# Kernel tuning notes

Hardware: AMD Instinct MI355X
Metric: run time of the kernel (lower is better)

Reference implementation:

```python
import jax, jax.numpy as jnp
import numpy as np

EMBED_DIM = 32
HIDDEN_DIM = 64
N = 1024
LN_EPS = 1e-5


def setup_inputs() -> dict:
    key = jax.random.key(0)
    ks = jax.random.split(key, 8)
    d, h = EMBED_DIM, HIDDEN_DIM
    s1 = 1.0 / np.sqrt(2 * d)
    s2 = 1.0 / np.sqrt(h)
    return {
        "node_embeddings": jax.random.normal(ks[0], (N, d), dtype=jnp.float32),
        # Linear(2d -> h), stored as (2d, h) for x @ W
        "W1": jax.random.uniform(ks[1], (2 * d, h), jnp.float32, -s1, s1),
        "b1": jnp.zeros((h,), jnp.float32),
        "g1": jnp.ones((h,), jnp.float32),
        "be1": jnp.zeros((h,), jnp.float32),
        "W2": jax.random.uniform(ks[2], (h, h), jnp.float32, -s2, s2),
        "b2": jnp.zeros((h,), jnp.float32),
        "g2": jnp.ones((h,), jnp.float32),
        "be2": jnp.zeros((h,), jnp.float32),
        "W3": jax.random.uniform(ks[3], (h, 1), jnp.float32, -s2, s2),
        "b3": jnp.zeros((1,), jnp.float32),
    }


def _layernorm(x, gamma, beta):
    mu = jnp.mean(x, axis=-1, keepdims=True)
    var = jnp.mean(jnp.square(x - mu), axis=-1, keepdims=True)
    return (x - mu) * jax.lax.rsqrt(var + LN_EPS) * gamma + beta


def reference(node_embeddings, W1, b1, g1, be1, W2, b2, g2, be2, W3, b3):
    n, d = node_embeddings.shape
    # pair_emb = cat([src_emb, dst_emb], -1); first linear applied without
    # materializing the concat: split W1 into src/dst halves.
    W1s, W1d = W1[:d], W1[d:]
    hs = node_embeddings @ W1s          # (N, h)
    hd = node_embeddings @ W1d          # (N, h)
    h = hs[:, None, :] + hd[None, :, :] + b1   # (N, N, h)
    h = jax.nn.relu(_layernorm(h, g1, be1))
    h = jax.nn.relu(_layernorm(h @ W2 + b2, g2, be2))
    out = jax.nn.sigmoid((h @ W3 + b3)[..., 0])  # (N, N)
    return out
```

## Files before the change

kernel.cpp:

```cpp
#include <hip/hip_runtime.h>
#include <hip/hip_bf16.h>

#define NN 1024
#define ED 32
#define HD 64
#define LN_EPS 1e-5f

typedef short bf16x8 __attribute__((ext_vector_type(8)));
typedef float f32x4 __attribute__((ext_vector_type(4)));

#define OFF_HS   0
#define OFF_HDB  65536
#define OFF_SS   131072
#define OFF_SD   132096
#define OFF_G1   133120
#define OFF_BE1  133184
#define OFF_B2   133248
#define OFF_G2   133312
#define OFF_BE2  133376
#define OFF_W3   133440
#define OFF_B3   133504
#define OFF_SB2  133505
#define OFF_W2F  133508

__device__ __forceinline__ bool buf_is_f32(const void* g1) {
  return *(const unsigned int*)g1 == 0x3F800000u;
}
template <bool F32>
__device__ __forceinline__ float ld(const void* p, int i) {
  return F32 ? ((const float*)p)[i]
             : __bfloat162float(((const __hip_bfloat16*)p)[i]);
}
__device__ __forceinline__ unsigned short f2bf(float f) {
  unsigned int b = __builtin_bit_cast(unsigned int, f);
  b += 0x7FFFu + ((b >> 16) & 1u);
  return (unsigned short)(b >> 16);
}
__device__ __forceinline__ unsigned int pack2bf(float a, float b) {
  return (unsigned int)f2bf(a) | ((unsigned int)f2bf(b) << 16);
}
__device__ __forceinline__ unsigned int pk_bf(float a, float b) {
  __hip_bfloat162 p = __float22bfloat162_rn(make_float2(a, b));
  unsigned int u;
  __builtin_memcpy(&u, &p, 4);
  return u;
}
__device__ __forceinline__ f32x4 splat4(float v) { f32x4 r = {v, v, v, v}; return r; }

template <int CTRL>
__device__ __forceinline__ float dpp_add(float v) {
  int m = __builtin_amdgcn_update_dpp(0, __builtin_bit_cast(int, v), CTRL, 0xF, 0xF, true);
  return v + __builtin_bit_cast(float, m);
}
__device__ __forceinline__ float red16(float v) {
  v = dpp_add<0xB1>(v);
  v = dpp_add<0x4E>(v);
  v = dpp_add<0x124>(v);
  v = dpp_add<0x128>(v);
  return v;
}

template <bool F32>
__device__ void prep_body(const void* E, const void* W1, const void* b1,
                          const void* g1, const void* be1, const void* W2,
                          const void* b2, const void* g2, const void* be2,
                          const void* W3, const void* b3, float* ws) {
  const int i = blockIdx.x, t = threadIdx.x;
  if (i < NN) {
    __shared__ float e[ED];
    if (t < ED) e[t] = ld<F32>(E, i * ED + t);
    __syncthreads();
    int k = t & 63;
    bool dside = t >= 64;
    int wofs = dside ? ED * HD : 0;
    float acc = 0.f;
#pragma unroll
    for (int c = 0; c < ED; ++c)
      acc = fmaf(e[c], ld<F32>(W1, wofs + c * HD + k), acc);
    if (dside) acc += ld<F32>(b1, k);
    float s = acc;
#pragma unroll
    for (int m = 1; m <= 32; m <<= 1) s += __shfl_xor(s, m);
    if (dside) {
      ws[OFF_HDB + i * HD + k] = acc;
      if (k == 0) ws[OFF_SD + i] = s;
    } else {
      ws[OFF_HS + i * HD + k] = acc;
      if (k == 0) ws[OFF_SS + i] = s;
    }
  } else if (i < NN + 16) {
    if (t < 32) {
      int d = (i - NN) * 32 + t;
      int lv = d & 63, nt = (d >> 6) & 3, kc = d >> 8;
      int k0 = kc * 32 + ((lv >> 4) & 3) * 8;
      int n = nt * 16 + (lv & 15);
      unsigned int u4[4];
#pragma unroll
      for (int jj = 0; jj < 4; ++jj)
        u4[jj] = pack2bf(ld<F32>(W2, (k0 + 2 * jj) * HD + n),
                         ld<F32>(W2, (k0 + 2 * jj + 1) * HD + n));
      ((uint4*)(ws + OFF_W2F))[d] = make_uint4(u4[0], u4[1], u4[2], u4[3]);
    }
  } else {
    __shared__ float rs[64];
    if (t < 64) {
      ws[OFF_G1  + t] = ld<F32>(g1,  t);
      ws[OFF_BE1 + t] = ld<F32>(be1, t);
      ws[OFF_B2  + t] = ld<F32>(b2,  t);
      ws[OFF_G2  + t] = ld<F32>(g2,  t);
      ws[OFF_BE2 + t] = ld<F32>(be2, t);
      ws[OFF_W3  + t] = ld<F32>(W3,  t);
      float s = 0.f;
      for (int n = 0; n < HD; ++n) s += ld<F32>(W2, t * HD + n);
      rs[t] = s;
    }
    if (t == 64) {
      float s = 0.f;
      for (int n = 0; n < HD; ++n) s += ld<F32>(b2, n);
      ws[OFF_SB2] = s;
    }
    if (t == 65) ws[OFF_B3] = ld<F32>(b3, 0);
    __syncthreads();
    unsigned short* st = (unsigned short*)(ws + OFF_W2F) + 4096;
    for (int s = t; s < 1024; s += 128) {
      int j = s & 7, lv = (s >> 3) & 63, kc = s >> 9;
      st[s] = f2bf(rs[kc * 32 + ((lv >> 4) & 3) * 8 + j]);
    }
  }
}

__global__ __launch_bounds__(128) void prep_kern(
    const void* E, const void* W1, const void* b1, const void* g1,
    const void* be1, const void* W2, const void* b2, const void* g2,
    const void* be2, const void* W3, const void* b3, float* ws) {
  if (buf_is_f32(g1))
    prep_body<true >(E, W1, b1, g1, be1, W2, b2, g2, be2, W3, b3, ws);
  else
    prep_body<false>(E, W1, b1, g1, be1, W2, b2, g2, be2, W3, b3, ws);
}

__global__ __launch_bounds__(256, 4) void pair_kern(
    const float* __restrict__ ws, float* __restrict__ out) {
  __shared__ float sh[1024];
  __shared__ float sdt[1024];
  __shared__ __align__(16) unsigned int X[256 * 32];
  const int t = threadIdx.x;
  const int bi = blockIdx.y, bj = blockIdx.x;
  const int l = t & 63, w = t >> 6;
  const int q = l >> 4, ln = l & 15;
  const float inv = 1.f / 64.f;

  {
    int r = t >> 4, c4 = t & 15;
    ((f32x4*)sh )[r * 16 + (c4 ^ r)] = ((const f32x4*)(ws + OFF_HS  + (bi * 16 + r) * HD))[c4];
    ((f32x4*)sdt)[r * 16 + (c4 ^ r)] = ((const f32x4*)(ws + OFF_HDB + (bj * 16 + r) * HD))[c4];
  }
  const int il = t >> 4, jl = t & 15;
  const float ssum = ws[OFF_SS + bi * 16 + il];
  const float dsum = ws[OFF_SD + bj * 16 + jl];
  __syncthreads();

  {
    const f32x4* A4 = (const f32x4*)sh;
    const f32x4* B4 = (const f32x4*)sdt;
    f32x4 xv[16];
    f32x4 q4 = splat4(0.f);
#pragma unroll
    for (int c = 0; c < 16; ++c) {
      f32x4 x = A4[il * 16 + (c ^ il)] + B4[jl * 16 + (c ^ jl)];
      xv[c] = x;
      q4 = __builtin_elementwise_fma(x, x, q4);
    }
    float ssq = (q4[0] + q4[1]) + (q4[2] + q4[3]);
    float mu = (ssum + dsum) * inv;
    float r1 = rsqrtf(fmaf(-mu, mu, ssq * inv) + LN_EPS);
    f32x4 r1v = splat4(r1), nm = splat4(-mu * r1), zero = splat4(0.f);
    uint4* Xr4 = (uint4*)(X + t * 32);
#pragma unroll
    for (int b = 0; b < 8; ++b) {
      unsigned int uu[4];
#pragma unroll
      for (int h = 0; h < 2; ++h) {
        int c = 2 * b + h;
        f32x4 g, be;
#pragma unroll
        for (int e = 0; e < 4; ++e) {
          g[e]  = ws[OFF_G1  + c * 4 + e];
          be[e] = ws[OFF_BE1 + c * 4 + e];
        }
        f32x4 u = __builtin_elementwise_fma(xv[c], r1v, nm);
        f32x4 v = __builtin_elementwise_fma(u, g, be);
        v = __builtin_elementwise_max(v, zero);
        uu[2 * h]     = pk_bf(v[0], v[1]);
        uu[2 * h + 1] = pk_bf(v[2], v[3]);
      }
      Xr4[b ^ (t & 7)] = make_uint4(uu[0], uu[1], uu[2], uu[3]);
    }
  }

  bf16x8 bf[2][4], bsum[2];
  const uint4* WF4 = (const uint4*)(ws + OFF_W2F);
#pragma unroll
  for (int kc = 0; kc < 2; ++kc) {
#pragma unroll
    for (int nt = 0; nt < 4; ++nt)
      bf[kc][nt] = __builtin_bit_cast(bf16x8, WF4[(kc * 4 + nt) * 64 + l]);
    bsum[kc] = __builtin_bit_cast(bf16x8, WF4[512 + kc * 64 + l]);
  }
  f32x4 acc[4][5];
  const uint4* XL = (const uint4*)X;
#pragma unroll
  for (int mt = 0; mt < 4; ++mt) {
    int m = w * 64 + mt * 16 + ln;
    bf16x8 a0 = __builtin_bit_cast(bf16x8, XL[m * 8 + (q ^ (m & 7))]);
    bf16x8 a1 = __builtin_bit_cast(bf16x8, XL[m * 8 + ((q + 4) ^ (m & 7))]);
#pragma unroll
    for (int nt = 0; nt < 5; ++nt) {
      bf16x8 b0  = (nt < 4) ? bf[0][nt] : bsum[0];
      bf16x8 b1f = (nt < 4) ? bf[1][nt] : bsum[1];
      f32x4 z4 = splat4(0.f);
      z4 = __builtin_amdgcn_mfma_f32_16x16x32_bf16(a0, b0, z4, 0, 0, 0);
      acc[mt][nt] = __builtin_amdgcn_mfma_f32_16x16x32_bf16(a1, b1f, z4, 0, 0, 0);
    }
  }

  float b2v[4], g2v[4], be2v[4], w3v[4];
#pragma unroll
  for (int nt = 0; nt < 4; ++nt) {
    int cix = nt * 16 + ln;
    b2v[nt]  = ws[OFF_B2  + cix];
    g2v[nt]  = ws[OFF_G2  + cix];
    be2v[nt] = ws[OFF_BE2 + cix];
    w3v[nt]  = ws[OFF_W3  + cix];
  }
  const float b3s = ws[OFF_B3];
  const float Sb2 = ws[OFF_SB2];

#pragma unroll
  for (int mt = 0; mt < 4; ++mt) {
    f32x4 y[4], qq = splat4(0.f);
#pragma unroll
    for (int nt = 0; nt < 4; ++nt) {
      y[nt] = acc[mt][nt] + splat4(b2v[nt]);
      qq = __builtin_elementwise_fma(y[nt], y[nt], qq);
    }
#pragma unroll
    for (int e = 0; e < 4; ++e) qq[e] = red16(qq[e]);
    f32x4 s4 = acc[mt][4] + splat4(Sb2);
    f32x4 mu = s4 * inv;
    f32x4 var = qq * inv - mu * mu;
    f32x4 r2;
#pragma unroll
    for (int e = 0; e < 4; ++e) r2[e] = rsqrtf(var[e] + LN_EPS);
    f32x4 z4 = splat4(0.f);
#pragma unroll
    for (int nt = 0; nt < 4; ++nt) {
      f32x4 u = (y[nt] - mu) * r2;
      f32x4 v = __builtin_elementwise_fma(u, splat4(g2v[nt]), splat4(be2v[nt]));
      v = __builtin_elementwise_max(v, splat4(0.f));
      z4 = __builtin_elementwise_fma(v, splat4(w3v[nt]), z4);
    }
#pragma unroll
    for (int e = 0; e < 4; ++e) z4[e] = red16(z4[e]);
    float z01 = (ln & 1) ? z4[1] : z4[0];
    float z23 = (ln & 1) ? z4[3] : z4[2];
    float zs = ((ln & 2) ? z23 : z01) + b3s;
    float o = 1.f / (1.f + __expf(-zs));
    if (ln < 4)
      out[(bi * 16 + w * 4 + mt) * NN + bj * 16 + q * 4 + ln] = o;
  }
}

extern "C" void kernel_launch(void* const* d_in, const int* in_sizes, int n_in,
                              void* d_out, int out_size, void* d_ws, size_t ws_size,
                              hipStream_t stream) {
  float* ws = (float*)d_ws;
  hipLaunchKernelGGL(prep_kern, dim3(NN + 17), dim3(128), 0, stream,
                     d_in[0], d_in[1], d_in[2], d_in[3], d_in[4], d_in[5],
                     d_in[6], d_in[7], d_in[8], d_in[9], d_in[10], ws);
  hipLaunchKernelGGL(pair_kern, dim3(64, 64), dim3(256), 0, stream,
                     ws, (float*)d_out);
}
```

Measured before the change: 118.9 us.

## Remap block grid, fold bias into MFMA init, and transpose-reduce final outputs

Launches a 1D grid and remaps block ids in strides of 8 so that neighbouring blocks spread their (bi,bj) tiles across groups, presumably to match XCD scheduling and cache locality. It seeds the MFMA accumulator with b2 and the row-sum bias, so the separate bias adds go away. The epilogue is fused per m-tile to reduce live accumulators, and the 16 per-lane partial sums go through a butterfly transpose-reduce with DPP moves. As a result every lane writes one output instead of 4 of 16 lanes doing redundant reductions. Uniform parameters are also loaded before the barrier.

```diff
diff --git a/kernel.cpp b/kernel.cpp
--- a/kernel.cpp
+++ b/kernel.cpp
@@ -51,6 +51,11 @@
 __device__ __forceinline__ float dpp_add(float v) {
   int m = __builtin_amdgcn_update_dpp(0, __builtin_bit_cast(int, v), CTRL, 0xF, 0xF, true);
   return v + __builtin_bit_cast(float, m);
+}
+template <int CTRL>
+__device__ __forceinline__ float dpp_mov(float v) {
+  return __builtin_bit_cast(float,
+      __builtin_amdgcn_update_dpp(0, __builtin_bit_cast(int, v), CTRL, 0xF, 0xF, true));
 }
 __device__ __forceinline__ float red16(float v) {
   v = dpp_add<0xB1>(v);
@@ -145,9 +150,12 @@
   __shared__ float sdt[1024];
   __shared__ __align__(16) unsigned int X[256 * 32];
   const int t = threadIdx.x;
-  const int bi = blockIdx.y, bj = blockIdx.x;
+  const int bid = blockIdx.x;
+  const int lid = (bid & 7) * 512 + (bid >> 3);
+  const int bi = lid >> 6, bj = lid & 63;
   const int l = t & 63, w = t >> 6;
   const int q = l >> 4, ln = l & 15;
+  const int il = t >> 4, jl = t & 15;
   const float inv = 1.f / 64.f;
 
   {
@@ -155,9 +163,19 @@
     ((f32x4*)sh )[r * 16 + (c4 ^ r)] = ((const f32x4*)(ws + OFF_HS  + (bi * 16 + r) * HD))[c4];
     ((f32x4*)sdt)[r * 16 + (c4 ^ r)] = ((const f32x4*)(ws + OFF_HDB + (bj * 16 + r) * HD))[c4];
   }
-  const int il = t >> 4, jl = t & 15;
   const float ssum = ws[OFF_SS + bi * 16 + il];
   const float dsum = ws[OFF_SD + bj * 16 + jl];
+  float b2v[4], g2v[4], be2v[4], w3v[4];
+#pragma unroll
+  for (int nt = 0; nt < 4; ++nt) {
+    int cix = nt * 16 + ln;
+    b2v[nt]  = ws[OFF_B2  + cix];
+    g2v[nt]  = ws[OFF_G2  + cix];
+    be2v[nt] = ws[OFF_BE2 + cix];
+    w3v[nt]  = ws[OFF_W3  + cix];
+  }
+  const float b3s = ws[OFF_B3];
+  const float Sb2 = ws[OFF_SB2];
   __syncthreads();
 
   {
@@ -207,67 +225,75 @@
       bf[kc][nt] = __builtin_bit_cast(bf16x8, WF4[(kc * 4 + nt) * 64 + l]);
     bsum[kc] = __builtin_bit_cast(bf16x8, WF4[512 + kc * 64 + l]);
   }
-  f32x4 acc[4][5];
   const uint4* XL = (const uint4*)X;
+  float zp[16];
 #pragma unroll
   for (int mt = 0; mt < 4; ++mt) {
     int m = w * 64 + mt * 16 + ln;
     bf16x8 a0 = __builtin_bit_cast(bf16x8, XL[m * 8 + (q ^ (m & 7))]);
     bf16x8 a1 = __builtin_bit_cast(bf16x8, XL[m * 8 + ((q + 4) ^ (m & 7))]);
+    f32x4 acc5[5];
 #pragma unroll
     for (int nt = 0; nt < 5; ++nt) {
       bf16x8 b0  = (nt < 4) ? bf[0][nt] : bsum[0];
       bf16x8 b1f = (nt < 4) ? bf[1][nt] : bsum[1];
-      f32x4 z4 = splat4(0.f);
+      f32x4 z4 = splat4(nt < 4 ? b2v[nt] : Sb2);
       z4 = __builtin_amdgcn_mfma_f32_16x16x32_bf16(a0, b0, z4, 0, 0, 0);
-      acc[mt][nt] = __builtin_amdgcn_mfma_f32_16x16x32_bf16(a1, b1f, z4, 0, 0, 0);
-    }
-  }
-
-  float b2v[4], g2v[4], be2v[4], w3v[4];
-#pragma unroll
-  for (int nt = 0; nt < 4; ++nt) {
-    int cix = nt * 16 + ln;
-    b2v[nt]  = ws[OFF_B2  + cix];
-    g2v[nt]  = ws[OFF_G2  + cix];
-    be2v[nt] = ws[OFF_BE2 + cix];
-    w3v[nt]  = ws[OFF_W3  + cix];
-  }
-  const float b3s = ws[OFF_B3];
-  const float Sb2 = ws[OFF_SB2];
-
-#pragma unroll
-  for (int mt = 0; mt < 4; ++mt) {
-    f32x4 y[4], qq = splat4(0.f);
+      acc5[nt] = __builtin_amdgcn_mfma_f32_16x16x32_bf16(a1, b1f, z4, 0, 0, 0);
+    }
+    f32x4 qq = splat4(0.f);
+#pragma unroll
+    for (int nt = 0; nt < 4; ++nt)
+      qq = __builtin_elementwise_fma(acc5[nt], acc5[nt], qq);
+#pragma unroll
+    for (int e = 0; e < 4; ++e) qq[e] = red16(qq[e]);
+    f32x4 mu = acc5[4] * splat4(inv);
+    f32x4 var = __builtin_elementwise_fma(qq, splat4(inv), -(mu * mu));
+    f32x4 r2;
+#pragma unroll
+    for (int e = 0; e < 4; ++e) r2[e] = rsqrtf(var[e] + LN_EPS);
+    f32x4 nm2 = -(mu * r2);
+    f32x4 z4 = splat4(0.f);
 #pragma unroll
     for (int nt = 0; nt < 4; ++nt) {
-      y[nt] = acc[mt][nt] + splat4(b2v[nt]);
-      qq = __builtin_elementwise_fma(y[nt], y[nt], qq);
-    }
-#pragma unroll
-    for (int e = 0; e < 4; ++e) qq[e] = red16(qq[e]);
-    f32x4 s4 = acc[mt][4] + splat4(Sb2);
-    f32x4 mu = s4 * inv;
-    f32x4 var = qq * inv - mu * mu;
-    f32x4 r2;
-#pragma unroll
-    for (int e = 0; e < 4; ++e) r2[e] = rsqrtf(var[e] + LN_EPS);
-    f32x4 z4 = splat4(0.f);
-#pragma unroll
-    for (int nt = 0; nt < 4; ++nt) {
-      f32x4 u = (y[nt] - mu) * r2;
+      f32x4 u = __builtin_elementwise_fma(acc5[nt], r2, nm2);
       f32x4 v = __builtin_elementwise_fma(u, splat4(g2v[nt]), splat4(be2v[nt]));
       v = __builtin_elementwise_max(v, splat4(0.f));
       z4 = __builtin_elementwise_fma(v, splat4(w3v[nt]), z4);
     }
 #pragma unroll
-    for (int e = 0; e < 4; ++e) z4[e] = red16(z4[e]);
-    float z01 = (ln & 1) ? z4[1] : z4[0];
-    float z23 = (ln & 1) ? z4[3] : z4[2];
-    float zs = ((ln & 2) ? z23 : z01) + b3s;
-    float o = 1.f / (1.f + __expf(-zs));
-    if (ln < 4)
-      out[(bi * 16 + w * 4 + mt) * NN + bj * 16 + q * 4 + ln] = o;
+    for (int e = 0; e < 4; ++e) zp[mt * 4 + e] = z4[e];
+  }
+
+  const bool p8 = (l & 8) != 0, p4b = (l & 4) != 0;
+  const bool p2b = (l & 2) != 0, p1b = (l & 1) != 0;
+  float s8v[8];
+#pragma unroll
+  for (int j = 0; j < 8; ++j) {
+    float kept = p8 ? zp[j + 8] : zp[j];
+    float disc = p8 ? zp[j] : zp[j + 8];
+    s8v[j] = kept + dpp_mov<0x128>(disc);
+  }
+  float s4v[4];
+#pragma unroll
+  for (int j = 0; j < 4; ++j) {
+    float kept = p4b ? s8v[j + 4] : s8v[j];
+    float disc = p4b ? s8v[j] : s8v[j + 4];
+    s4v[j] = kept + dpp_mov<0x141>(disc);
+  }
+  float s2v[2];
+#pragma unroll
+  for (int j = 0; j < 2; ++j) {
+    float kept = p2b ? s4v[j + 2] : s4v[j];
+    float disc = p2b ? s4v[j] : s4v[j + 2];
+    s2v[j] = kept + dpp_mov<0x4E>(disc);
+  }
+  {
+    float kept = p1b ? s2v[1] : s2v[0];
+    float disc = p1b ? s2v[0] : s2v[1];
+    float zfin = kept + dpp_mov<0xB1>(disc);
+    float o = 1.f / (1.f + __expf(-(zfin + b3s)));
+    out[(bi * 16 + w * 4 + (ln >> 2)) * NN + bj * 16 + q * 4 + (ln & 3)] = o;
   }
 }
 
@@ -278,6 +304,6 @@
   hipLaunchKernelGGL(prep_kern, dim3(NN + 17), dim3(128), 0, stream,
                      d_in[0], d_in[1], d_in[2], d_in[3], d_in[4], d_in[5],
                      d_in[6], d_in[7], d_in[8], d_in[9], d_in[10], ws);
-  hipLaunchKernelGGL(pair_kern, dim3(64, 64), dim3(256), 0, stream,
+  hipLaunchKernelGGL(pair_kern, dim3(4096), dim3(256), 0, stream,
                      ws, (float*)d_out);
 }
```

New measurement: 134.2 us. 1.13x slower.
